# Performance work log

Measured on AMD Instinct MI355X. Metric: run time of the kernel, lower is better.

Reference implementation:

```python
import jax, jax.numpy as jnp
import numpy as np

NUM_CLASSES = 2
KS = 5  # kernel_size
EPS = 1e-8  # torch cosine_similarity eps


def setup_inputs() -> dict:
    key = jax.random.key(0)
    k1, k2, k3 = jax.random.split(key, 3)
    b, c, h, w = 8, 256, 128, 128
    er_input = jax.random.normal(k1, (b, c, h, w), dtype=jnp.float32)
    seg_label = jax.random.randint(k2, (b, h, w), 0, 2, dtype=jnp.int32)
    gt_boundary_seg = jax.random.randint(k3, (b, h, w), 0, 2, dtype=jnp.int32)
    return {"er_input": er_input, "seg_label": seg_label, "gt_boundary_seg": gt_boundary_seg}


def _context_loss(er_input, seg_label, gt_boundary_seg):
    # seg_label / gt_boundary_seg already at er_input spatial size (nearest interp is identity)
    b, c, h, w = er_input.shape
    r = KS // 2
    seg0 = jnp.where(seg_label == 255, 0, seg_label)
    gtb0 = jnp.where(gt_boundary_seg == 255, 0, gt_boundary_seg)
    gt_b = gtb0 * seg0                                  # [b,h,w] boundary pixels on fg classes
    interior = jnp.zeros((h, w), bool).at[r:h - r, r:w - r].set(True)
    valid = (gt_b > 0) & interior                       # pixels whose 5x5 window is in-bounds
    include = (gt_b > 0).any(axis=(1, 2))               # images contributing to scale_num
    cnt = valid.sum(axis=(1, 2)).astype(er_input.dtype)  # [b]

    norm = jnp.maximum(jnp.sqrt((er_input * er_input).sum(axis=1)), EPS)  # [b,h,w]
    validf = valid.astype(er_input.dtype)
    total = jnp.zeros((b,), dtype=er_input.dtype)
    n_shift = 0
    for dy in range(-r, r + 1):
        for dx in range(-r, r + 1):
            if dy == 0 and dx == 0:
                continue
            n_shift += 1
            # value at p+ (dy,dx) brought to p; valid pixels are interior so no wrap issue
            feat_s = jnp.roll(er_input, (-dy, -dx), axis=(2, 3))
            norm_s = jnp.roll(norm, (-dy, -dx), axis=(1, 2))
            seg_s = jnp.roll(seg_label, (-dy, -dx), axis=(1, 2))
            dot = (er_input * feat_s).sum(axis=1)       # [b,h,w]
            cos = dot / (norm * norm_s)
            # one_hot(seg,256)[:num_classes] dot product == labels equal AND label < num_classes
            labsim = ((seg_label == seg_s) & (seg_label < NUM_CLASSES)).astype(er_input.dtype)
            sq = (cos - labsim) ** 2
            # mse_loss over selected boundary pixels of image i
            total = total + (sq * validf).sum(axis=(1, 2)) / jnp.maximum(cnt, 1.0)
    loss_i = total / float(n_shift)                     # per-image context_loss_pi / 24
    scale_num = jnp.maximum(include.sum(), 1)
    return (loss_i * include.astype(loss_i.dtype)).sum() / scale_num.astype(loss_i.dtype)


def reference(er_input, seg_label, gt_boundary_seg):
    return _context_loss(er_input, seg_label, gt_boundary_seg)
```

## Files before the change

kernel.cpp:

```cpp
#include <hip/hip_runtime.h>
#include <math.h>

#define BATCH 8
#define CH    256
#define H     128
#define W     128
#define PLANE (H * W)
#define NPIX  (BATCH * PLANE)
#define NSHIFT 12
#define NMAPS  13
#define NCHUNK 4
#define CPC    (CH / NCHUNK)
#define CSTRIDE (NMAPS * NPIX)

static __device__ __constant__ int S_DY[NSHIFT] = {0,0,1,1,1,1,1,2,2,2,2,2};
static __device__ __constant__ int S_DX[NSHIFT] = {1,2,-2,-1,0,1,2,-2,-1,0,1,2};

#define NCORRB (BATCH * 32 * NCHUNK)
#define NSTATB (BATCH * 64)

__device__ __forceinline__ void fma4(float& acc, const float4& a, const float4& b) {
    acc = fmaf(a.x, b.x, acc);
    acc = fmaf(a.y, b.y, acc);
    acc = fmaf(a.z, b.z, acc);
    acc = fmaf(a.w, b.w, acc);
}

__global__ __launch_bounds__(64) void k_prep(int* __restrict__ cnt,
                                             int* __restrict__ inc,
                                             float* __restrict__ out) {
    int t = threadIdx.x;
    if (t < 8) { cnt[t] = 0; inc[t] = 0; }
    if (t == 0) out[0] = 0.0f;
}

__global__ __launch_bounds__(256, 4) void k_corr(const float* __restrict__ er,
                                                 const int* __restrict__ seg,
                                                 const int* __restrict__ gtb,
                                                 float* __restrict__ comb,
                                                 int* __restrict__ cnt,
                                                 int* __restrict__ inc) {
    __shared__ float4 lds[6][132];
    int t = threadIdx.x;

    if (blockIdx.x >= NCORRB) {
        int blk2 = blockIdx.x - NCORRB;
        int b = blk2 >> 6;
        int i = (blk2 & 63) * 256 + t;
        int my_cnt = 0, my_any = 0;
        {
            int s = seg[b * PLANE + i];
            int g = gtb[b * PLANE + i];
            int s0 = (s == 255) ? 0 : s;
            int g0 = (g == 255) ? 0 : g;
            if (s0 > 0 && g0 > 0) {
                my_any = 1;
                int y = i >> 7, x = i & 127;
                if (y >= 2 && y < H - 2 && x >= 2 && x < W - 2) my_cnt = 1;
            }
        }
        for (int o = 32; o > 0; o >>= 1) {
            my_cnt += __shfl_down(my_cnt, o, 64);
            my_any |= __shfl_down(my_any, o, 64);
        }
        __shared__ int sc[4], sa[4];
        int lane = t & 63, wid = t >> 6;
        if (lane == 0) { sc[wid] = my_cnt; sa[wid] = my_any; }
        __syncthreads();
        if (t == 0) {
            int c = sc[0] + sc[1] + sc[2] + sc[3];
            int a = sa[0] | sa[1] | sa[2] | sa[3];
            if (c) atomicAdd(&cnt[b], c);
            if (a) atomicOr(&inc[b], 1);
        }
        return;
    }

    int blk = blockIdx.x;
    int chunk = blk & 3;
    int tile  = (blk >> 2) & 31;
    int b     = blk >> 7;
    int y0 = tile * 4;
    int c0 = chunk * CPC;
    int r = t >> 7;
    int x = t & 127;

    if (t < 24) {
        int row = t >> 2, col = t & 3;
        int xs = (col < 2) ? col : (col + 128);
        lds[row][xs] = make_float4(0.f, 0.f, 0.f, 0.f);
    }

    float accA[13], accB[13];
#pragma unroll
    for (int i = 0; i < 13; i++) { accA[i] = 0.0f; accB[i] = 0.0f; }

    const float* base = er + (size_t)b * CH * PLANE;

    float pf[3][4];
    auto load_quad = [&](int c) {
#pragma unroll
        for (int k = 0; k < 3; ++k) {
            int s = t + k * 256;
            int row = s >> 7;
            int xs = s & 127;
            int y = y0 + row;
            if (y < H) {
                const float* p0 = base + (size_t)c * PLANE + y * W + xs;
                pf[k][0] = p0[0];
                pf[k][1] = p0[PLANE];
                pf[k][2] = p0[2 * PLANE];
                pf[k][3] = p0[3 * PLANE];
            } else {
                pf[k][0] = 0.f; pf[k][1] = 0.f; pf[k][2] = 0.f; pf[k][3] = 0.f;
            }
        }
    };

    load_quad(c0);
    const int iters = CPC / 4;
    for (int it = 0; it < iters; ++it) {
        __syncthreads();
#pragma unroll
        for (int k = 0; k < 3; ++k) {
            int s = t + k * 256;
            int row = s >> 7;
            int xs = s & 127;
            lds[row][xs + 2] = make_float4(pf[k][0], pf[k][1], pf[k][2], pf[k][3]);
        }
        __syncthreads();
        if (it + 1 < iters) load_quad(c0 + 4 * (it + 1));

        const float4* lp = &lds[2 * r][x + 2];
        float4 cA = lp[0];
        float4 cB = lp[132];
        {
            float4 v1 = lp[1], v2 = lp[2];
            fma4(accA[0], cA, cA);
            fma4(accA[1], cA, v1);
            fma4(accA[2], cA, v2);
        }
        {
            float4 m2 = lp[130], m1 = lp[131], p1 = lp[133], p2 = lp[134];
            fma4(accA[3], cA, m2);
            fma4(accA[4], cA, m1);
            fma4(accA[5], cA, cB);
            fma4(accA[6], cA, p1);
            fma4(accA[7], cA, p2);
            fma4(accB[0], cB, cB);
            fma4(accB[1], cB, p1);
            fma4(accB[2], cB, p2);
        }
        {
            float4 m2 = lp[262], m1 = lp[263], v0 = lp[264], p1 = lp[265], p2 = lp[266];
            fma4(accA[8],  cA, m2);
            fma4(accA[9],  cA, m1);
            fma4(accA[10], cA, v0);
            fma4(accA[11], cA, p1);
            fma4(accA[12], cA, p2);
            fma4(accB[3], cB, m2);
            fma4(accB[4], cB, m1);
            fma4(accB[5], cB, v0);
            fma4(accB[6], cB, p1);
            fma4(accB[7], cB, p2);
        }
        {
            float4 m2 = lp[394], m1 = lp[395], v0 = lp[396], p1 = lp[397], p2 = lp[398];
            fma4(accB[8],  cB, m2);
            fma4(accB[9],  cB, m1);
            fma4(accB[10], cB, v0);
            fma4(accB[11], cB, p1);
            fma4(accB[12], cB, p2);
        }
    }

    float* cb = comb + (size_t)chunk * CSTRIDE;
    int pixA = b * PLANE + (y0 + 2 * r) * W + x;
    int pixB = pixA + W;
#pragma unroll
    for (int m = 0; m < NSHIFT; ++m) {
        cb[m * NPIX + pixA] = accA[m + 1];
        cb[m * NPIX + pixB] = accB[m + 1];
    }
    cb[NSHIFT * NPIX + pixA] = accA[0];
    cb[NSHIFT * NPIX + pixB] = accB[0];
}

__device__ __forceinline__ float sum4c(const float* __restrict__ p) {
    return (p[0] + p[CSTRIDE]) + (p[2 * CSTRIDE] + p[3 * CSTRIDE]);
}

__global__ __launch_bounds__(256) void k_loss(const float* __restrict__ comb,
                                              const int* __restrict__ seg,
                                              const int* __restrict__ gtb,
                                              const int* __restrict__ cnt,
                                              const int* __restrict__ inc,
                                              float* __restrict__ out) {
    const float* dots   = comb;
    const float* normsq = comb + NSHIFT * NPIX;
    int idx = blockIdx.x * 256 + threadIdx.x;
    int b = idx >> 14;
    int rem = idx & (PLANE - 1);
    int y = rem >> 7;
    int x = rem & 127;

    int sn = 0;
#pragma unroll
    for (int b2 = 0; b2 < BATCH; b2++) sn += (inc[b2] != 0);
    if (sn < 1) sn = 1;
    int cb = cnt[b]; if (cb < 1) cb = 1;
    float factor = inc[b] ? 1.0f / (24.0f * (float)cb * (float)sn) : 0.0f;

    float val = 0.0f;
    if (y >= 2 && y < H - 2 && x >= 2 && x < W - 2) {
        int sp = seg[idx];
        int gp = gtb[idx];
        int s0 = (sp == 255) ? 0 : sp;
        int g0 = (gp == 255) ? 0 : gp;
        if (s0 > 0 && g0 > 0) {
            float np = fmaxf(sqrtf(sum4c(normsq + idx)), 1e-8f);
            float sum = 0.0f;
#pragma unroll
            for (int i = 0; i < NSHIFT; ++i) {
                int off = S_DY[i] * W + S_DX[i];
                {
                    float d  = sum4c(dots + i * NPIX + idx);
                    float nn = fmaxf(sqrtf(sum4c(normsq + idx + off)), 1e-8f);
                    float cosv = d / (np * nn);
                    int sq = seg[idx + off];
                    float lab = (sp == sq && sp < 2) ? 1.0f : 0.0f;
                    float tt = cosv - lab;
                    sum = fmaf(tt, tt, sum);
                }
                {
                    float d  = sum4c(dots + i * NPIX + idx - off);
                    float nn = fmaxf(sqrtf(sum4c(normsq + idx - off)), 1e-8f);
                    float cosv = d / (np * nn);
                    int sq = seg[idx - off];
                    float lab = (sp == sq && sp < 2) ? 1.0f : 0.0f;
                    float tt = cosv - lab;
                    sum = fmaf(tt, tt, sum);
                }
            }
            val = sum * factor;
        }
    }

    for (int o = 32; o > 0; o >>= 1)
        val += __shfl_down(val, o, 64);
    __shared__ float wsum[4];
    int lane = threadIdx.x & 63;
    int wid  = threadIdx.x >> 6;
    if (lane == 0) wsum[wid] = val;
    __syncthreads();
    if (threadIdx.x == 0) {
        float s = wsum[0] + wsum[1] + wsum[2] + wsum[3];
        atomicAdd(out, s);
    }
}

extern "C" void kernel_launch(void* const* d_in, const int* in_sizes, int n_in,
                              void* d_out, int out_size, void* d_ws, size_t ws_size,
                              hipStream_t stream) {
    const float* er  = (const float*)d_in[0];
    const int*   seg = (const int*)d_in[1];
    const int*   gtb = (const int*)d_in[2];
    float* out = (float*)d_out;

    float* ws   = (float*)d_ws;
    float* comb = ws;
    int*   cnt  = (int*)(comb + NCHUNK * CSTRIDE);
    int*   inc  = cnt + 8;

    hipLaunchKernelGGL(k_prep, dim3(1), dim3(64), 0, stream, cnt, inc, out);
    hipLaunchKernelGGL(k_corr, dim3(NCORRB + NSTATB), dim3(256), 0, stream,
                       er, seg, gtb, comb, cnt, inc);
    hipLaunchKernelGGL(k_loss, dim3(NPIX / 256), dim3(256), 0, stream,
                       comb, seg, gtb, cnt, inc, out);
}
```

Measured before the change: 221.5 us.

## Double-buffer LDS in correlation kernel, taller tiles, precompute reciprocal norms

The correlation kernel now uses 512-thread blocks covering 8-row tiles, which reduces halo reloads. It also double-buffers the shared-memory channel tiles, so each iteration needs one barrier instead of two. A new small kernel precomputes clamped reciprocal norms per pixel. The loss kernel then uses one multiply instead of repeated 4-chunk norm sums, sqrt and division for each neighbour. The changes add an extra launch and an extra NPIX buffer, use more LDS per block, and replace the exact sqrt/divide with rsqrt, which may slightly change precision.

```diff
diff --git a/kernel.cpp b/kernel.cpp
--- a/kernel.cpp
+++ b/kernel.cpp
@@ -16,8 +16,10 @@
 static __device__ __constant__ int S_DY[NSHIFT] = {0,0,1,1,1,1,1,2,2,2,2,2};
 static __device__ __constant__ int S_DX[NSHIFT] = {1,2,-2,-1,0,1,2,-2,-1,0,1,2};
 
-#define NCORRB (BATCH * 32 * NCHUNK)
-#define NSTATB (BATCH * 64)
+#define TROWS  8
+#define NTILE  (H / TROWS)
+#define NCORRB (BATCH * NTILE * NCHUNK)
+#define NSTATB (BATCH * 32)
 
 __device__ __forceinline__ void fma4(float& acc, const float4& a, const float4& b) {
     acc = fmaf(a.x, b.x, acc);
@@ -34,19 +36,19 @@
     if (t == 0) out[0] = 0.0f;
 }
 
-__global__ __launch_bounds__(256, 4) void k_corr(const float* __restrict__ er,
+__global__ __launch_bounds__(512, 4) void k_corr(const float* __restrict__ er,
                                                  const int* __restrict__ seg,
                                                  const int* __restrict__ gtb,
                                                  float* __restrict__ comb,
                                                  int* __restrict__ cnt,
                                                  int* __restrict__ inc) {
-    __shared__ float4 lds[6][132];
+    __shared__ float4 lds[2][10][132];
     int t = threadIdx.x;
 
     if (blockIdx.x >= NCORRB) {
         int blk2 = blockIdx.x - NCORRB;
-        int b = blk2 >> 6;
-        int i = (blk2 & 63) * 256 + t;
+        int b = blk2 >> 5;
+        int i = (blk2 & 31) * 512 + t;
         int my_cnt = 0, my_any = 0;
         {
             int s = seg[b * PLANE + i];
@@ -63,13 +65,14 @@
             my_cnt += __shfl_down(my_cnt, o, 64);
             my_any |= __shfl_down(my_any, o, 64);
         }
-        __shared__ int sc[4], sa[4];
+        __shared__ int sc[8], sa[8];
         int lane = t & 63, wid = t >> 6;
         if (lane == 0) { sc[wid] = my_cnt; sa[wid] = my_any; }
         __syncthreads();
         if (t == 0) {
-            int c = sc[0] + sc[1] + sc[2] + sc[3];
-            int a = sa[0] | sa[1] | sa[2] | sa[3];
+            int c = 0, a = 0;
+#pragma unroll
+            for (int w2 = 0; w2 < 8; ++w2) { c += sc[w2]; a |= sa[w2]; }
             if (c) atomicAdd(&cnt[b], c);
             if (a) atomicOr(&inc[b], 1);
         }
@@ -78,17 +81,18 @@
 
     int blk = blockIdx.x;
     int chunk = blk & 3;
-    int tile  = (blk >> 2) & 31;
-    int b     = blk >> 7;
-    int y0 = tile * 4;
+    int tile  = (blk >> 2) & 15;
+    int b     = blk >> 6;
+    int y0 = tile * TROWS;
     int c0 = chunk * CPC;
     int r = t >> 7;
     int x = t & 127;
 
-    if (t < 24) {
-        int row = t >> 2, col = t & 3;
+    if (t < 80) {
+        int bi = t / 40, rem = t % 40;
+        int row = rem >> 2, col = rem & 3;
         int xs = (col < 2) ? col : (col + 128);
-        lds[row][xs] = make_float4(0.f, 0.f, 0.f, 0.f);
+        lds[bi][row][xs] = make_float4(0.f, 0.f, 0.f, 0.f);
     }
 
     float accA[13], accB[13];
@@ -101,37 +105,46 @@
     auto load_quad = [&](int c) {
 #pragma unroll
         for (int k = 0; k < 3; ++k) {
-            int s = t + k * 256;
-            int row = s >> 7;
-            int xs = s & 127;
-            int y = y0 + row;
-            if (y < H) {
-                const float* p0 = base + (size_t)c * PLANE + y * W + xs;
-                pf[k][0] = p0[0];
-                pf[k][1] = p0[PLANE];
-                pf[k][2] = p0[2 * PLANE];
-                pf[k][3] = p0[3 * PLANE];
-            } else {
-                pf[k][0] = 0.f; pf[k][1] = 0.f; pf[k][2] = 0.f; pf[k][3] = 0.f;
+            if (k < 2 || t < 256) {
+                int s = t + k * 512;
+                int row = s >> 7;
+                int xs = s & 127;
+                int y = y0 + row;
+                if (y < H) {
+                    const float* p0 = base + (size_t)c * PLANE + y * W + xs;
+                    pf[k][0] = p0[0];
+                    pf[k][1] = p0[PLANE];
+                    pf[k][2] = p0[2 * PLANE];
+                    pf[k][3] = p0[3 * PLANE];
+                } else {
+                    pf[k][0] = 0.f; pf[k][1] = 0.f; pf[k][2] = 0.f; pf[k][3] = 0.f;
+                }
             }
         }
     };
-
+    auto commit_quad = [&](int bi) {
+#pragma unroll
+        for (int k = 0; k < 3; ++k) {
+            if (k < 2 || t < 256) {
+                int s = t + k * 512;
+                int row = s >> 7;
+                int xs = s & 127;
+                lds[bi][row][xs + 2] = make_float4(pf[k][0], pf[k][1], pf[k][2], pf[k][3]);
+            }
+        }
+    };
+
+    const int iters = CPC / 4;
     load_quad(c0);
-    const int iters = CPC / 4;
-    for (int it = 0; it < iters; ++it) {
+    commit_quad(0);
+    load_quad(c0 + 4);
+
+    auto iter = [&](int it, int cur) {
         __syncthreads();
-#pragma unroll
-        for (int k = 0; k < 3; ++k) {
-            int s = t + k * 256;
-            int row = s >> 7;
-            int xs = s & 127;
-            lds[row][xs + 2] = make_float4(pf[k][0], pf[k][1], pf[k][2], pf[k][3]);
-        }
-        __syncthreads();
-        if (it + 1 < iters) load_quad(c0 + 4 * (it + 1));
-
-        const float4* lp = &lds[2 * r][x + 2];
+        if (it + 1 < iters) commit_quad(cur ^ 1);
+        if (it + 2 < iters) load_quad(c0 + 4 * (it + 2));
+
+        const float4* lp = &lds[cur][2 * r][x + 2];
         float4 cA = lp[0];
         float4 cB = lp[132];
         {
@@ -172,6 +185,11 @@
             fma4(accB[11], cB, p1);
             fma4(accB[12], cB, p2);
         }
+    };
+
+    for (int it = 0; it < iters; it += 2) {
+        iter(it, 0);
+        iter(it + 1, 1);
     }
 
     float* cb = comb + (size_t)chunk * CSTRIDE;
@@ -186,18 +204,26 @@
     cb[NSHIFT * NPIX + pixB] = accB[0];
 }
 
+__global__ __launch_bounds__(256) void k_rn(const float* __restrict__ comb,
+                                            float* __restrict__ rn) {
+    int idx = blockIdx.x * 256 + threadIdx.x;
+    const float* ns = comb + NSHIFT * NPIX;
+    float s = (ns[idx] + ns[idx + CSTRIDE]) + (ns[idx + 2 * CSTRIDE] + ns[idx + 3 * CSTRIDE]);
+    rn[idx] = fminf(rsqrtf(s), 1e8f);
+}
+
 __device__ __forceinline__ float sum4c(const float* __restrict__ p) {
     return (p[0] + p[CSTRIDE]) + (p[2 * CSTRIDE] + p[3 * CSTRIDE]);
 }
 
 __global__ __launch_bounds__(256) void k_loss(const float* __restrict__ comb,
+                                              const float* __restrict__ rn,
                                               const int* __restrict__ seg,
                                               const int* __restrict__ gtb,
                                               const int* __restrict__ cnt,
                                               const int* __restrict__ inc,
                                               float* __restrict__ out) {
-    const float* dots   = comb;
-    const float* normsq = comb + NSHIFT * NPIX;
+    const float* dots = comb;
     int idx = blockIdx.x * 256 + threadIdx.x;
     int b = idx >> 14;
     int rem = idx & (PLANE - 1);
@@ -218,15 +244,14 @@
         int s0 = (sp == 255) ? 0 : sp;
         int g0 = (gp == 255) ? 0 : gp;
         if (s0 > 0 && g0 > 0) {
-            float np = fmaxf(sqrtf(sum4c(normsq + idx)), 1e-8f);
+            float npr = rn[idx];
             float sum = 0.0f;
 #pragma unroll
             for (int i = 0; i < NSHIFT; ++i) {
                 int off = S_DY[i] * W + S_DX[i];
                 {
                     float d  = sum4c(dots + i * NPIX + idx);
-                    float nn = fmaxf(sqrtf(sum4c(normsq + idx + off)), 1e-8f);
-                    float cosv = d / (np * nn);
+                    float cosv = d * (npr * rn[idx + off]);
                     int sq = seg[idx + off];
                     float lab = (sp == sq && sp < 2) ? 1.0f : 0.0f;
                     float tt = cosv - lab;
@@ -234,8 +259,7 @@
                 }
                 {
                     float d  = sum4c(dots + i * NPIX + idx - off);
-                    float nn = fmaxf(sqrtf(sum4c(normsq + idx - off)), 1e-8f);
-                    float cosv = d / (np * nn);
+                    float cosv = d * (npr * rn[idx - off]);
                     int sq = seg[idx - off];
                     float lab = (sp == sq && sp < 2) ? 1.0f : 0.0f;
                     float tt = cosv - lab;
@@ -269,12 +293,14 @@
 
     float* ws   = (float*)d_ws;
     float* comb = ws;
-    int*   cnt  = (int*)(comb + NCHUNK * CSTRIDE);
+    float* rn   = comb + NCHUNK * CSTRIDE;
+    int*   cnt  = (int*)(rn + NPIX);
     int*   inc  = cnt + 8;
 
     hipLaunchKernelGGL(k_prep, dim3(1), dim3(64), 0, stream, cnt, inc, out);
-    hipLaunchKernelGGL(k_corr, dim3(NCORRB + NSTATB), dim3(256), 0, stream,
+    hipLaunchKernelGGL(k_corr, dim3(NCORRB + NSTATB), dim3(512), 0, stream,
                        er, seg, gtb, comb, cnt, inc);
+    hipLaunchKernelGGL(k_rn, dim3(NPIX / 256), dim3(256), 0, stream, comb, rn);
     hipLaunchKernelGGL(k_loss, dim3(NPIX / 256), dim3(256), 0, stream,
-                       comb, seg, gtb, cnt, inc, out);
-}
+                       comb, rn, seg, gtb, cnt, inc, out);
+}
```

New measurement: 215.7 us. 1.03x faster.
